# Optimization experiments

Hardware: AMD Instinct MI355X
Metric: run time of the kernel (lower is better)

## Reference

```python
import jax, jax.numpy as jnp
import numpy as np
import math

NUM_HEADS = 8
DIM_Q = 512
DIM_K = 512
DIM_V = 512
EPS = 1e-5


def _layernorm(x, g, b):
    mu = jnp.mean(x, axis=-1, keepdims=True)
    var = jnp.mean(jnp.square(x - mu), axis=-1, keepdims=True)
    return (x - mu) * jax.lax.rsqrt(var + EPS) * g + b


def setup_inputs() -> dict:
    key = jax.random.key(0)
    ks = jax.random.split(key, 16)
    B, Nq, Nk = 8, 1024, 1024
    s_q = 1.0 / math.sqrt(DIM_Q)
    s_v = 1.0 / math.sqrt(DIM_V)
    return {
        "Q": jax.random.normal(ks[0], (B, Nq, DIM_Q), jnp.float32),
        "K": jax.random.normal(ks[1], (B, Nk, DIM_K), jnp.float32),
        "Wq": jax.random.uniform(ks[2], (DIM_Q, DIM_V), jnp.float32, -s_q, s_q),
        "bq": jax.random.uniform(ks[3], (DIM_V,), jnp.float32, -s_q, s_q),
        "Wk": jax.random.uniform(ks[4], (DIM_K, DIM_V), jnp.float32, -s_q, s_q),
        "bk": jax.random.uniform(ks[5], (DIM_V,), jnp.float32, -s_q, s_q),
        "Wv": jax.random.uniform(ks[6], (DIM_K, DIM_V), jnp.float32, -s_q, s_q),
        "bv": jax.random.uniform(ks[7], (DIM_V,), jnp.float32, -s_q, s_q),
        "Wo": jax.random.uniform(ks[8], (DIM_V, DIM_V), jnp.float32, -s_v, s_v),
        "bo": jax.random.uniform(ks[9], (DIM_V,), jnp.float32, -s_v, s_v),
        "g0": jnp.ones((DIM_V,), jnp.float32),
        "b0": jnp.zeros((DIM_V,), jnp.float32),
        "g1": jnp.ones((DIM_V,), jnp.float32),
        "b1": jnp.zeros((DIM_V,), jnp.float32),
        "M": jax.random.randint(ks[10], (B, Nq, Nk), 0, 2, jnp.int32),
    }


def reference(Q, K, Wq, bq, Wk, bk, Wv, bv, Wo, bo, g0, b0, g1, b1, M):
    B, Nq, _ = Q.shape
    Nk = K.shape[1]
    H = NUM_HEADS
    d = DIM_V // H
    # projections
    Qp = Q @ Wq + bq                      # [B,Nq,Dv]
    Kp = K @ Wk + bk                      # [B,Nk,Dv]
    Vp = K @ Wv + bv                      # [B,Nk,Dv]
    # split heads: channel h*d+j -> head h (matches torch split/cat ordering)
    Qh = Qp.reshape(B, Nq, H, d)
    Kh = Kp.reshape(B, Nk, H, d)
    Vh = Vp.reshape(B, Nk, H, d)
    # scores scaled by sqrt(dim_V) (faithful to original, NOT sqrt(head_dim))
    A = jnp.einsum("bqhd,bkhd->bhqk", Qh, Kh) / math.sqrt(DIM_V)
    A = jnp.where(M[:, None, :, :] == 0, -jnp.inf, A)
    A = jax.nn.softmax(A, axis=-1)
    # residual add of the (projected, per-head) query, then merge heads
    O = Qh + jnp.einsum("bhqk,bkhd->bqhd", A, Vh)
    O = O.reshape(B, Nq, DIM_V)
    O = _layernorm(O, g0, b0)
    O = O + jax.nn.relu(O @ Wo + bo)
    O = _layernorm(O, g1, b1)
    return O
```

## Files before the change

kernel.cpp:

```cpp
#include <hip/hip_runtime.h>

typedef unsigned short u16;
typedef unsigned int u32;
typedef unsigned long long u64;
typedef __attribute__((ext_vector_type(8))) short short8;
typedef __attribute__((ext_vector_type(4))) float f32x4;
typedef __attribute__((ext_vector_type(4))) u32 u32x4;

#define BATCH 8
#define NSEQ 1024
#define DMODEL 512
#define HDIM 64
#define SCALE_LOG2E 0.06375871114929199f
#define FIXED_MAX 16.0f

#define O_QBF 0ULL
#define O_KBF 8388608ULL
#define O_WB  16777216ULL
#define O_QP  19922944ULL
#define O_KP  28311552ULL
#define O_VP  36700160ULL

__device__ __forceinline__ u16 f2bf(float f) {
  u32 u = __float_as_uint(f);
  u = (u + 0x7fffu + ((u >> 16) & 1u)) >> 16;
  return (u16)u;
}
__device__ __forceinline__ float bf2f(u16 s) {
  return __uint_as_float(((u32)s) << 16);
}
__device__ __forceinline__ void gload16(const void* g, void* l) {
  __builtin_amdgcn_global_load_lds((const __attribute__((address_space(1))) void*)g,
                                   (__attribute__((address_space(3))) void*)l, 16, 0, 0);
}
__device__ __forceinline__ u32 cvtpk(float a, float b) {
  u32 r;
  asm("v_cvt_pk_bf16_f32 %0, %1, %2" : "=v"(r) : "v"(a), "v"(b));
  return r;
}

__global__ __launch_bounds__(256) void prep_kernel(
    const float* __restrict__ Q, const float* __restrict__ K,
    const float* __restrict__ Wq, const float* __restrict__ Wk,
    const float* __restrict__ Wv, const float* __restrict__ Wo,
    const int* __restrict__ M,
    u16* __restrict__ Qbf, u16* __restrict__ Kbf, u16* __restrict__ Wb,
    u16* __restrict__ Mbias)
{
  __shared__ float lds[64 * 68];
  const int bi = blockIdx.x, t = threadIdx.x;
  if (bi < 4096) {
    const float* src = (bi < 2048) ? Q : K;
    u16* dst = (bi < 2048) ? Qbf : Kbf;
    const int lb = bi & 2047;
    const size_t base = ((size_t)lb * 256 + t) * 8;
    float4 a = *(const float4*)(src + base);
    float4 c = *(const float4*)(src + base + 4);
    short8 o;
    o[0] = (short)f2bf(a.x); o[1] = (short)f2bf(a.y);
    o[2] = (short)f2bf(a.z); o[3] = (short)f2bf(a.w);
    o[4] = (short)f2bf(c.x); o[5] = (short)f2bf(c.y);
    o[6] = (short)f2bf(c.z); o[7] = (short)f2bf(c.w);
    *(short8*)(dst + base) = o;
  } else if (bi < 4352) {
    const int qid = bi - 4096;
    const int w = qid >> 6;
    const int tt = qid & 63;
    const int tr = tt >> 3, tc = tt & 7;
    const float* W = (w == 0) ? Wq : (w == 1) ? Wk : (w == 2) ? Wv : Wo;
#pragma unroll
    for (int j = 0; j < 4; ++j) {
      int vi = j * 256 + t;
      int row = vi >> 4, c4 = vi & 15;
      float4 v = *(const float4*)(W + (size_t)(tr * 64 + row) * 512 + tc * 64 + c4 * 4);
      lds[row * 68 + c4 * 4 + 0] = v.x;
      lds[row * 68 + c4 * 4 + 1] = v.y;
      lds[row * 68 + c4 * 4 + 2] = v.z;
      lds[row * 68 + c4 * 4 + 3] = v.w;
    }
    __syncthreads();
#pragma unroll
    for (int j = 0; j < 2; ++j) {
      int oi = j * 256 + t;
      int nl = oi >> 3, k8 = oi & 7;
      short8 o;
#pragma unroll
      for (int i = 0; i < 8; ++i) o[i] = (short)f2bf(lds[(k8 * 8 + i) * 68 + nl]);
      *(short8*)(Wb + (size_t)w * 262144 + (size_t)(tc * 64 + nl) * 512 + tr * 64 + k8 * 8) = o;
    }
  } else {
    const int pb = bi - 4352;
    const size_t idx = ((size_t)pb * 256 + t) * 16;
    const int4* Ms = (const int4*)(M + idx);
    int4 m0 = Ms[0], m1 = Ms[1], m2 = Ms[2], m3 = Ms[3];
    int mv[16] = {m0.x, m0.y, m0.z, m0.w, m1.x, m1.y, m1.z, m1.w,
                  m2.x, m2.y, m2.z, m2.w, m3.x, m3.y, m3.z, m3.w};
    short8 o0, o1;
#pragma unroll
    for (int i = 0; i < 8; ++i) {
      o0[i] = mv[i] ? (short)0 : (short)0xC700;
      o1[i] = mv[8 + i] ? (short)0 : (short)0xC700;
    }
    *(short8*)(Mbias + idx) = o0;
    *(short8*)(Mbias + idx + 8) = o1;
  }
}

template<int MODE>
__global__ __launch_bounds__(256) void gemm_bt(
    const u16* __restrict__ Aq, const u16* __restrict__ Ak,
    const u16* __restrict__ Wb,
    const float* __restrict__ b0, const float* __restrict__ b1, const float* __restrict__ b2,
    u16* __restrict__ outp, const u16* __restrict__ resid)
{
  __shared__ __align__(16) char Alds[8192];
  __shared__ __align__(16) char Blds[8192];
  const int tid = threadIdx.x;
  const int wv = tid >> 6, lane = tid & 63;
  const int g16 = lane >> 4, l16 = lane & 15;
  const int wr = wv >> 1, wc = wv & 1;
  const int bx = blockIdx.x, by = blockIdx.y, bz = blockIdx.z;

  const u16* A; const u16* W; const float* bias; u16* out;
  if (MODE == 0) {
    A = (bz == 0) ? Aq : Ak;
    W = Wb + (size_t)bz * 262144;
    bias = (bz == 0) ? b0 : ((bz == 1) ? b1 : b2);
    out = outp + (size_t)bz * 4194304;
  } else {
    A = Aq; W = Wb; bias = b0; out = outp;
  }

  const int m0 = bx * 128, n0 = by * 128;
  f32x4 acc[4][4] = {};

  for (int kt = 0; kt < 16; ++kt) {
    const int k0 = kt * 32;
#pragma unroll
    for (int r = 0; r < 2; ++r) {
      int idx = r * 256 + tid;
      int row = idx >> 2, sl = idx & 3;
      gload16(A + (size_t)(m0 + row) * 512 + k0 + sl * 8, Alds + r * 4096 + wv * 1024);
      gload16(W + (size_t)(n0 + row) * 512 + k0 + sl * 8, Blds + r * 4096 + wv * 1024);
    }
    __syncthreads();
    short8 af[4], bfr[4];
#pragma unroll
    for (int mt = 0; mt < 4; ++mt)
      af[mt] = *(const short8*)(Alds + (wr * 64 + mt * 16 + l16) * 64 + g16 * 16);
#pragma unroll
    for (int nt = 0; nt < 4; ++nt)
      bfr[nt] = *(const short8*)(Blds + (wc * 64 + nt * 16 + l16) * 64 + g16 * 16);
#pragma unroll
    for (int mt = 0; mt < 4; ++mt)
#pragma unroll
      for (int nt = 0; nt < 4; ++nt)
        acc[mt][nt] = __builtin_amdgcn_mfma_f32_16x16x32_bf16(af[mt], bfr[nt], acc[mt][nt], 0, 0, 0);
    __syncthreads();
  }

#pragma unroll
  for (int nt = 0; nt < 4; ++nt) {
    int col = n0 + wc * 64 + nt * 16 + l16;
    float bcol = bias[col];
#pragma unroll
    for (int mt = 0; mt < 4; ++mt) {
#pragma unroll
      for (int r = 0; r < 4; ++r) {
        int row = m0 + wr * 64 + mt * 16 + g16 * 4 + r;
        float v = acc[mt][nt][r] + bcol;
        if (MODE == 1) {
          v = fmaxf(v, 0.f) + bf2f(resid[(size_t)row * 512 + col]);
        }
        out[(size_t)row * 512 + col] = f2bf(v);
      }
    }
  }
}

__global__ __launch_bounds__(256, 4) void attn_kernel(
    const u16* __restrict__ Qp, const u16* __restrict__ Kp, const u16* __restrict__ Vp,
    const u16* __restrict__ Mbias, u16* __restrict__ O1)
{
  __shared__ __align__(16) char K_lds[2][8192];
  __shared__ __align__(16) char VT_lds[2][8192];

  const int tid = threadIdx.x;
  const int wv = tid >> 6, lane = tid & 63;
  const int g16 = lane >> 4, l16 = lane & 15;
  const int l7 = l16 & 7;

  const int wg = blockIdx.x;
  const int swz = (wg & 7) * 128 + (wg >> 3);
  const int qt = swz & 15;
  const int h = (swz >> 4) & 7;
  const int b = swz >> 7;
  const int qg = qt * 64;
  const int hb = h * HDIM;
  const size_t batch_row = (size_t)b * NSEQ;

  const int q = qg + wv * 16 + l16;
  const int dv2 = (tid & 31) * 2;
  const int kg = tid >> 5;
  const int v_kc = kg >> 2, v_gg = kg & 3;

  short8 b_q[2];
#pragma unroll
  for (int c = 0; c < 2; ++c) {
    short8 raw = *(const short8*)(Qp + (batch_row + q) * DMODEL + hb + c * 32 + g16 * 8);
    short8 sc;
#pragma unroll
    for (int j = 0; j < 8; ++j) sc[j] = (short)f2bf(bf2f((u16)raw[j]) * SCALE_LOG2E);
    b_q[c] = sc;
  }

  const u64* Mq = (const u64*)(Mbias + (batch_row + q) * 1024);

  auto stageK = [&](int kt2, char* dst) {
#pragma unroll
    for (int r = 0; r < 2; ++r) {
      int idx = r * 256 + tid;
      int row = idx >> 3, sl = idx & 7;
      int chunk = sl ^ (row & 7);
      gload16(Kp + (batch_row + kt2 * 64 + row) * DMODEL + hb + chunk * 8,
              dst + r * 4096 + wv * 1024);
    }
  };
  auto loadV = [&](int kt2, u32 (&vr)[8]) {
#pragma unroll
    for (int j = 0; j < 8; ++j) {
      int row = v_kc * 32 + (j >> 2) * 16 + v_gg * 4 + (j & 3);
      vr[j] = *(const u32*)(Vp + (batch_row + kt2 * 64 + row) * DMODEL + hb + dv2);
    }
  };
  auto writeVT = [&](const u32 (&vr)[8], char* dstv) {
    u32x4 lo, hi;
#pragma unroll
    for (int i = 0; i < 4; ++i) {
      lo[i] = __builtin_amdgcn_perm(vr[2 * i + 1], vr[2 * i], 0x05040100u);
      hi[i] = __builtin_amdgcn_perm(vr[2 * i + 1], vr[2 * i], 0x07060302u);
    }
    *(u32x4*)(dstv + dv2 * 128 + ((kg ^ (dv2 & 7)) << 4)) = lo;
    *(u32x4*)(dstv + (dv2 + 1) * 128 + ((kg ^ ((dv2 + 1) & 7)) << 4)) = hi;
  };

  float lL = 0.f;
  f32x4 accO[4] = {};

  u32 vreg[8];
  u64 biasA[4], biasB[4];

  stageK(0, &K_lds[0][0]);
  loadV(0, vreg);
#pragma unroll
  for (int kf = 0; kf < 4; ++kf) biasA[kf] = Mq[kf * 4 + g16];
  writeVT(vreg, &VT_lds[0][0]);
  loadV(1, vreg);

#define ATTN_TILE(KT, CUR, BIN, BOUT)                                          \
  do {                                                                         \
    asm volatile("s_waitcnt vmcnt(12) lgkmcnt(0)" ::: "memory");               \
    __builtin_amdgcn_sched_barrier(0);                                         \
    __builtin_amdgcn_s_barrier();                                              \
    __builtin_amdgcn_sched_barrier(0);                                         \
    char* Kc = &K_lds[CUR][0];                                                 \
    char* Vc = &VT_lds[CUR][0];                                                \
    if ((KT) < 15) {                                                           \
      writeVT(vreg, &VT_lds[(CUR) ^ 1][0]);                                    \
      stageK((KT) + 1, &K_lds[(CUR) ^ 1][0]);                                  \
      loadV((KT) + 2 < 16 ? (KT) + 2 : 15, vreg);                              \
      _Pragma("unroll")                                                        \
      for (int kf = 0; kf < 4; ++kf)                                           \
        BOUT[kf] = Mq[((KT) + 1) * 16 + kf * 4 + g16];                         \
    }                                                                          \
    f32x4 s_[4];                                                               \
    __builtin_amdgcn_s_setprio(1);                                             \
    _Pragma("unroll")                                                          \
    for (int kf = 0; kf < 4; ++kf) {                                           \
      int row = kf * 16 + l16;                                                 \
      short8 ak0 = *(const short8*)(Kc + row * 128 + ((g16 ^ l7) << 4));       \
      short8 ak1 = *(const short8*)(Kc + row * 128 + (((4 + g16) ^ l7) << 4)); \
      u64 bv = BIN[kf];                                                        \
      u32 blo = (u32)bv, bhi = (u32)(bv >> 32);                                \
      f32x4 acc;                                                               \
      acc[0] = __uint_as_float(blo << 16);                                     \
      acc[1] = __uint_as_float(blo & 0xffff0000u);                             \
      acc[2] = __uint_as_float(bhi << 16);                                     \
      acc[3] = __uint_as_float(bhi & 0xffff0000u);                             \
      acc = __builtin_amdgcn_mfma_f32_16x16x32_bf16(ak0, b_q[0], acc, 0, 0, 0);\
      acc = __builtin_amdgcn_mfma_f32_16x16x32_bf16(ak1, b_q[1], acc, 0, 0, 0);\
      s_[kf] = acc;                                                            \
    }                                                                          \
    __builtin_amdgcn_s_setprio(0);                                             \
    float sum = 0.f;                                                           \
    u32 c0a[4], c1a[4];                                                        \
    _Pragma("unroll")                                                          \
    for (int kf = 0; kf < 4; ++kf) {                                           \
      float e0 = __builtin_amdgcn_exp2f(s_[kf][0] - FIXED_MAX);                \
      float e1 = __builtin_amdgcn_exp2f(s_[kf][1] - FIXED_MAX);                \
      float e2 = __builtin_amdgcn_exp2f(s_[kf][2] - FIXED_MAX);                \
      float e3 = __builtin_amdgcn_exp2f(s_[kf][3] - FIXED_MAX);                \
      sum += (e0 + e1) + (e2 + e3);                                            \
      c0a[kf] = cvtpk(e0, e1);                                                 \
      c1a[kf] = cvtpk(e2, e3);                                                 \
    }                                                                          \
    lL += sum;                                                                 \
    u32x4 t0 = {c0a[0], c1a[0], c0a[1], c1a[1]};                               \
    u32x4 t1 = {c0a[2], c1a[2], c0a[3], c1a[3]};                               \
    short8 b_p0 = *(short8*)&t0;                                               \
    short8 b_p1 = *(short8*)&t1;                                               \
    __builtin_amdgcn_s_setprio(1);                                             \
    _Pragma("unroll")                                                          \
    for (int f = 0; f < 4; ++f) {                                              \
      int vrow = f * 16 + l16;                                                 \
      short8 av0 = *(const short8*)(Vc + vrow * 128 + ((g16 ^ l7) << 4));      \
      short8 av1 = *(const short8*)(Vc + vrow * 128 + (((4 + g16) ^ l7) << 4));\
      accO[f] = __builtin_amdgcn_mfma_f32_16x16x32_bf16(av0, b_p0, accO[f], 0, 0, 0); \
      accO[f] = __builtin_amdgcn_mfma_f32_16x16x32_bf16(av1, b_p1, accO[f], 0, 0, 0); \
    }                                                                          \
    __builtin_amdgcn_s_setprio(0);                                             \
  } while (0)

  for (int t = 0; t < 8; ++t) {
    ATTN_TILE(2 * t, 0, biasA, biasB);
    ATTN_TILE(2 * t + 1, 1, biasB, biasA);
  }
#undef ATTN_TILE

  float l = lL;
  l += __shfl_xor(l, 16, 64);
  l += __shfl_xor(l, 32, 64);
  float inv = 1.0f / fmaxf(l, 1e-20f);
#pragma unroll
  for (int f = 0; f < 4; ++f) {
    size_t o = (batch_row + q) * DMODEL + hb + f * 16 + g16 * 4;
    u64 qh = *(const u64*)(Qp + o);
    u64 ov = 0;
#pragma unroll
    for (int r = 0; r < 4; ++r) {
      float val = accO[f][r] * inv + bf2f((u16)(qh >> (r * 16)));
      ov |= ((u64)f2bf(val)) << (r * 16);
    }
    *(u64*)(O1 + o) = ov;
  }
}

template<int OUTF>
__global__ __launch_bounds__(256) void ln_kernel(
    const u16* __restrict__ X, const float* __restrict__ g, const float* __restrict__ bb,
    void* __restrict__ outv)
{
  const int tid = threadIdx.x;
  const int wv = tid >> 6, lane = tid & 63;
  const size_t row = (size_t)blockIdx.x * 4 + wv;
  short8 x8 = *(const short8*)(X + row * 512 + lane * 8);
  float xf[8];
  float s = 0.f, s2 = 0.f;
#pragma unroll
  for (int i = 0; i < 8; ++i) {
    xf[i] = bf2f((u16)x8[i]);
    s += xf[i];
    s2 += xf[i] * xf[i];
  }
#pragma unroll
  for (int d = 1; d < 64; d <<= 1) {
    s += __shfl_xor(s, d, 64);
    s2 += __shfl_xor(s2, d, 64);
  }
  float mu = s * (1.f / 512.f);
  float var = s2 * (1.f / 512.f) - mu * mu;
  float rs = rsqrtf(var + 1e-5f);
  float4 ga = *(const float4*)(g + lane * 8);
  float4 gb = *(const float4*)(g + lane * 8 + 4);
  float4 ba = *(const float4*)(bb + lane * 8);
  float4 bc = *(const float4*)(bb + lane * 8 + 4);
  float gv[8] = {ga.x, ga.y, ga.z, ga.w, gb.x, gb.y, gb.z, gb.w};
  float bv[8] = {ba.x, ba.y, ba.z, ba.w, bc.x, bc.y, bc.z, bc.w};
  float y[8];
#pragma unroll
  for (int i = 0; i < 8; ++i) y[i] = (xf[i] - mu) * rs * gv[i] + bv[i];
  if (OUTF) {
    float* o = (float*)outv + row * 512 + lane * 8;
    float4 o1 = {y[0], y[1], y[2], y[3]};
    float4 o2 = {y[4], y[5], y[6], y[7]};
    *(float4*)o = o1;
    *(float4*)(o + 4) = o2;
  } else {
    short8 o;
#pragma unroll
    for (int i = 0; i < 8; ++i) o[i] = (short)f2bf(y[i]);
    *(short8*)((u16*)outv + row * 512 + lane * 8) = o;
  }
}

extern "C" void kernel_launch(void* const* d_in, const int* in_sizes, int n_in,
                              void* d_out, int out_size, void* d_ws, size_t ws_size,
                              hipStream_t stream) {
  (void)in_sizes; (void)n_in; (void)out_size; (void)ws_size;
  const float* Q  = (const float*)d_in[0];
  const float* K  = (const float*)d_in[1];
  const float* Wq = (const float*)d_in[2];
  const float* bq = (const float*)d_in[3];
  const float* Wk = (const float*)d_in[4];
  const float* bk = (const float*)d_in[5];
  const float* Wv = (const float*)d_in[6];
  const float* bv = (const float*)d_in[7];
  const float* Wo = (const float*)d_in[8];
  const float* bo = (const float*)d_in[9];
  const float* g0 = (const float*)d_in[10];
  const float* b0 = (const float*)d_in[11];
  const float* g1 = (const float*)d_in[12];
  const float* b1 = (const float*)d_in[13];
  const int*   M  = (const int*)d_in[14];
  float* out = (float*)d_out;
  char* ws = (char*)d_ws;

  u16* Qbf = (u16*)(ws + O_QBF);
  u16* Kbf = (u16*)(ws + O_KBF);
  u16* Wb  = (u16*)(ws + O_WB);
  u16* Qp  = (u16*)(ws + O_QP);
  u16* Kp  = (u16*)(ws + O_KP);
  u16* Vp  = (u16*)(ws + O_VP);
  u16* Mbias = (u16*)d_out;
  u16* O1  = Kbf;
  u16* Xn  = Qp;
  u16* Z   = Qbf;

  prep_kernel<<<6400, 256, 0, stream>>>(Q, K, Wq, Wk, Wv, Wo, M, Qbf, Kbf, Wb, Mbias);
  gemm_bt<0><<<dim3(64, 4, 3), 256, 0, stream>>>(Qbf, Kbf, Wb, bq, bk, bv, Qp, nullptr);
  attn_kernel<<<1024, 256, 0, stream>>>(Qp, Kp, Vp, Mbias, O1);
  ln_kernel<0><<<2048, 256, 0, stream>>>(O1, g0, b0, (void*)Xn);
  gemm_bt<1><<<dim3(64, 4, 1), 256, 0, stream>>>(Xn, nullptr, Wb + 3 * 262144, bo,
                                                 nullptr, nullptr, Z, Xn);
  ln_kernel<1><<<2048, 256, 0, stream>>>(Z, g1, b1, (void*)out);
}
```

Measured before the change: 118.4 us.

## Process two key tiles per barrier in attention with doubled LDS buffers

The attention loop now stages two 64-key K/V tiles per iteration into LDS buffers of twice the size. This halves the number of workgroup barriers and waitcnt points and lets more global loads sit in flight. In exchange, LDS per block doubles to 64KB, the launch-bounds occupancy hint drops from 4 to 2, and register use rises from the extra V staging registers and bias arrays, so fewer waves may be resident per CU.

```diff
diff --git a/kernel.cpp b/kernel.cpp
--- a/kernel.cpp
+++ b/kernel.cpp
@@ -178,12 +178,12 @@
   }
 }
 
-__global__ __launch_bounds__(256, 4) void attn_kernel(
+__global__ __launch_bounds__(256, 2) void attn_kernel(
     const u16* __restrict__ Qp, const u16* __restrict__ Kp, const u16* __restrict__ Vp,
     const u16* __restrict__ Mbias, u16* __restrict__ O1)
 {
-  __shared__ __align__(16) char K_lds[2][8192];
-  __shared__ __align__(16) char VT_lds[2][8192];
+  __shared__ __align__(16) char K_lds[2][16384];
+  __shared__ __align__(16) char VT_lds[2][16384];
 
   const int tid = threadIdx.x;
   const int wv = tid >> 6, lane = tid & 63;
@@ -247,40 +247,33 @@
   float lL = 0.f;
   f32x4 accO[4] = {};
 
-  u32 vreg[8];
-  u64 biasA[4], biasB[4];
+  u32 v0[8], v1[8];
+  u64 biasA[8], biasB[8];
 
   stageK(0, &K_lds[0][0]);
-  loadV(0, vreg);
-#pragma unroll
-  for (int kf = 0; kf < 4; ++kf) biasA[kf] = Mq[kf * 4 + g16];
-  writeVT(vreg, &VT_lds[0][0]);
-  loadV(1, vreg);
-
-#define ATTN_TILE(KT, CUR, BIN, BOUT)                                          \
+  stageK(1, &K_lds[0][8192]);
+  loadV(0, v0);
+  loadV(1, v1);
+#pragma unroll
+  for (int kf = 0; kf < 4; ++kf) {
+    biasA[kf] = Mq[kf * 4 + g16];
+    biasA[4 + kf] = Mq[16 + kf * 4 + g16];
+  }
+  writeVT(v0, &VT_lds[0][0]);
+  writeVT(v1, &VT_lds[0][8192]);
+  loadV(2, v0);
+  loadV(3, v1);
+
+#define SUBTILE(KCP, VCP, BARR, BOFF)                                          \
   do {                                                                         \
-    asm volatile("s_waitcnt vmcnt(12) lgkmcnt(0)" ::: "memory");               \
-    __builtin_amdgcn_sched_barrier(0);                                         \
-    __builtin_amdgcn_s_barrier();                                              \
-    __builtin_amdgcn_sched_barrier(0);                                         \
-    char* Kc = &K_lds[CUR][0];                                                 \
-    char* Vc = &VT_lds[CUR][0];                                                \
-    if ((KT) < 15) {                                                           \
-      writeVT(vreg, &VT_lds[(CUR) ^ 1][0]);                                    \
-      stageK((KT) + 1, &K_lds[(CUR) ^ 1][0]);                                  \
-      loadV((KT) + 2 < 16 ? (KT) + 2 : 15, vreg);                              \
-      _Pragma("unroll")                                                        \
-      for (int kf = 0; kf < 4; ++kf)                                           \
-        BOUT[kf] = Mq[((KT) + 1) * 16 + kf * 4 + g16];                         \
-    }                                                                          \
     f32x4 s_[4];                                                               \
     __builtin_amdgcn_s_setprio(1);                                             \
     _Pragma("unroll")                                                          \
     for (int kf = 0; kf < 4; ++kf) {                                           \
       int row = kf * 16 + l16;                                                 \
-      short8 ak0 = *(const short8*)(Kc + row * 128 + ((g16 ^ l7) << 4));       \
-      short8 ak1 = *(const short8*)(Kc + row * 128 + (((4 + g16) ^ l7) << 4)); \
-      u64 bv = BIN[kf];                                                        \
+      short8 ak0 = *(const short8*)((KCP) + row * 128 + ((g16 ^ l7) << 4));    \
+      short8 ak1 = *(const short8*)((KCP) + row * 128 + (((4 + g16) ^ l7) << 4)); \
+      u64 bv = BARR[(BOFF) + kf];                                              \
       u32 blo = (u32)bv, bhi = (u32)(bv >> 32);                                \
       f32x4 acc;                                                               \
       acc[0] = __uint_as_float(blo << 16);                                     \
@@ -313,19 +306,51 @@
     _Pragma("unroll")                                                          \
     for (int f = 0; f < 4; ++f) {                                              \
       int vrow = f * 16 + l16;                                                 \
-      short8 av0 = *(const short8*)(Vc + vrow * 128 + ((g16 ^ l7) << 4));      \
-      short8 av1 = *(const short8*)(Vc + vrow * 128 + (((4 + g16) ^ l7) << 4));\
+      short8 av0 = *(const short8*)((VCP) + vrow * 128 + ((g16 ^ l7) << 4));   \
+      short8 av1 = *(const short8*)((VCP) + vrow * 128 + (((4 + g16) ^ l7) << 4)); \
       accO[f] = __builtin_amdgcn_mfma_f32_16x16x32_bf16(av0, b_p0, accO[f], 0, 0, 0); \
       accO[f] = __builtin_amdgcn_mfma_f32_16x16x32_bf16(av1, b_p1, accO[f], 0, 0, 0); \
     }                                                                          \
     __builtin_amdgcn_s_setprio(0);                                             \
   } while (0)
 
-  for (int t = 0; t < 8; ++t) {
-    ATTN_TILE(2 * t, 0, biasA, biasB);
-    ATTN_TILE(2 * t + 1, 1, biasB, biasA);
-  }
-#undef ATTN_TILE
+#define ATTN_IT(IT, CUR, BIN, BOUT, VMCSTR)                                    \
+  do {                                                                         \
+    asm volatile("s_waitcnt vmcnt(" VMCSTR ") lgkmcnt(0)" ::: "memory");       \
+    __builtin_amdgcn_sched_barrier(0);                                         \
+    __builtin_amdgcn_s_barrier();                                              \
+    __builtin_amdgcn_sched_barrier(0);                                         \
+    char* Kc = &K_lds[CUR][0];                                                 \
+    char* Vc = &VT_lds[CUR][0];                                                \
+    if ((IT) < 7) {                                                            \
+      writeVT(v0, &VT_lds[(CUR) ^ 1][0]);                                      \
+      writeVT(v1, &VT_lds[(CUR) ^ 1][8192]);                                   \
+      stageK(2 * (IT) + 2, &K_lds[(CUR) ^ 1][0]);                              \
+      stageK(2 * (IT) + 3, &K_lds[(CUR) ^ 1][8192]);                           \
+    }                                                                          \
+    if ((IT) < 6) {                                                            \
+      loadV(2 * (IT) + 4, v0);                                                 \
+      loadV(2 * (IT) + 5, v1);                                                 \
+    }                                                                          \
+    if ((IT) < 7) {                                                            \
+      _Pragma("unroll")                                                        \
+      for (int kf = 0; kf < 4; ++kf) {                                         \
+        BOUT[kf] = Mq[(2 * (IT) + 2) * 16 + kf * 4 + g16];                     \
+        BOUT[4 + kf] = Mq[(2 * (IT) + 3) * 16 + kf * 4 + g16];                 \
+      }                                                                        \
+    }                                                                          \
+    SUBTILE(Kc, Vc, BIN, 0);                                                   \
+    SUBTILE(Kc + 8192, Vc + 8192, BIN, 4);                                     \
+  } while (0)
+
+  for (int t = 0; t < 3; ++t) {
+    ATTN_IT(2 * t, 0, biasA, biasB, "24");
+    ATTN_IT(2 * t + 1, 1, biasB, biasA, "24");
+  }
+  ATTN_IT(6, 0, biasA, biasB, "24");
+  ATTN_IT(7, 1, biasB, biasA, "8");
+#undef ATTN_IT
+#undef SUBTILE
 
   float l = lL;
   l += __shfl_xor(l, 16, 64);
```

New measurement: 117.1 us. No clear change (-1.1%).

## Pack attention mask into bitmask and remap GEMM blocks across XCDs

Applied to the files above, without the earlier changes.

The prep kernel now turns the int32 mask into a 1-bit-per-key bitmask via wave ballots, in place of a bf16 bias array the size of the full score matrix. The attention kernel reads one u64 per 64-key tile and expands the bits into the additive bias in registers. This cuts mask traffic in the attention kernel by a factor of 16 and shrinks the prep writes. The GEMM launches also become 1D with an XCD-aware block remap for better L2 locality. The cost is more per-element select work in the inner loop and a serial 32-iteration ballot loop per wave in prep.

```diff
diff --git a/kernel.cpp b/kernel.cpp
--- a/kernel.cpp
+++ b/kernel.cpp
@@ -17,6 +17,7 @@
 #define O_QBF 0ULL
 #define O_KBF 8388608ULL
 #define O_WB  16777216ULL
+#define O_MB  18874368ULL
 #define O_QP  19922944ULL
 #define O_KP  28311552ULL
 #define O_VP  36700160ULL
@@ -45,7 +46,7 @@
     const float* __restrict__ Wv, const float* __restrict__ Wo,
     const int* __restrict__ M,
     u16* __restrict__ Qbf, u16* __restrict__ Kbf, u16* __restrict__ Wb,
-    u16* __restrict__ Mbias)
+    u64* __restrict__ Mb)
 {
   __shared__ float lds[64 * 68];
   const int bi = blockIdx.x, t = threadIdx.x;
@@ -90,19 +91,16 @@
     }
   } else {
     const int pb = bi - 4352;
-    const size_t idx = ((size_t)pb * 256 + t) * 16;
-    const int4* Ms = (const int4*)(M + idx);
-    int4 m0 = Ms[0], m1 = Ms[1], m2 = Ms[2], m3 = Ms[3];
-    int mv[16] = {m0.x, m0.y, m0.z, m0.w, m1.x, m1.y, m1.z, m1.w,
-                  m2.x, m2.y, m2.z, m2.w, m3.x, m3.y, m3.z, m3.w};
-    short8 o0, o1;
-#pragma unroll
-    for (int i = 0; i < 8; ++i) {
-      o0[i] = mv[i] ? (short)0 : (short)0xC700;
-      o1[i] = mv[8 + i] ? (short)0 : (short)0xC700;
-    }
-    *(short8*)(Mbias + idx) = o0;
-    *(short8*)(Mbias + idx + 8) = o1;
+    const int wv = t >> 6, lane = t & 63;
+    for (int i = 0; i < 32; ++i) {
+      int widx = pb * 128 + wv * 32 + i;
+      int kc = widx & 15;
+      int qq = (widx >> 4) & 1023;
+      int bb = widx >> 14;
+      int mv = M[((size_t)bb * 1024 + qq) * 1024 + kc * 64 + lane];
+      u64 bal = __ballot(mv != 0);
+      if (lane == 0) Mb[widx] = bal;
+    }
   }
 }
 
@@ -119,7 +117,13 @@
   const int wv = tid >> 6, lane = tid & 63;
   const int g16 = lane >> 4, l16 = lane & 15;
   const int wr = wv >> 1, wc = wv & 1;
-  const int bx = blockIdx.x, by = blockIdx.y, bz = blockIdx.z;
+
+  const int p = blockIdx.x;
+  const int xcd = p & 7, rest = p >> 3;
+  const int bx = xcd + ((rest & 7) << 3);
+  const int q2 = rest >> 3;
+  const int by = (MODE == 0) ? (q2 & 3) : q2;
+  const int bz = (MODE == 0) ? (q2 >> 2) : 0;
 
   const u16* A; const u16* W; const float* bias; u16* out;
   if (MODE == 0) {
@@ -180,7 +184,7 @@
 
 __global__ __launch_bounds__(256, 4) void attn_kernel(
     const u16* __restrict__ Qp, const u16* __restrict__ Kp, const u16* __restrict__ Vp,
-    const u16* __restrict__ Mbias, u16* __restrict__ O1)
+    const u64* __restrict__ Mb, u16* __restrict__ O1)
 {
   __shared__ __align__(16) char K_lds[2][8192];
   __shared__ __align__(16) char VT_lds[2][8192];
@@ -214,7 +218,7 @@
     b_q[c] = sc;
   }
 
-  const u64* Mq = (const u64*)(Mbias + (batch_row + q) * 1024);
+  const u64* Mq = Mb + (batch_row + q) * 16;
 
   auto stageK = [&](int kt2, char* dst) {
 #pragma unroll
@@ -248,18 +252,17 @@
   f32x4 accO[4] = {};
 
   u32 vreg[8];
-  u64 biasA[4], biasB[4];
+  u64 mksA, mksB;
 
   stageK(0, &K_lds[0][0]);
   loadV(0, vreg);
-#pragma unroll
-  for (int kf = 0; kf < 4; ++kf) biasA[kf] = Mq[kf * 4 + g16];
+  mksA = Mq[0];
   writeVT(vreg, &VT_lds[0][0]);
   loadV(1, vreg);
 
-#define ATTN_TILE(KT, CUR, BIN, BOUT)                                          \
+#define ATTN_TILE(KT, CUR, MKS, MKSN)                                          \
   do {                                                                         \
-    asm volatile("s_waitcnt vmcnt(12) lgkmcnt(0)" ::: "memory");               \
+    asm volatile("s_waitcnt vmcnt(8) lgkmcnt(0)" ::: "memory");                \
     __builtin_amdgcn_sched_barrier(0);                                         \
     __builtin_amdgcn_s_barrier();                                              \
     __builtin_amdgcn_sched_barrier(0);                                         \
@@ -269,9 +272,7 @@
       writeVT(vreg, &VT_lds[(CUR) ^ 1][0]);                                    \
       stageK((KT) + 1, &K_lds[(CUR) ^ 1][0]);                                  \
       loadV((KT) + 2 < 16 ? (KT) + 2 : 15, vreg);                              \
-      _Pragma("unroll")                                                        \
-      for (int kf = 0; kf < 4; ++kf)                                           \
-        BOUT[kf] = Mq[((KT) + 1) * 16 + kf * 4 + g16];                         \
+      MKSN = Mq[(KT) + 1];                                                     \
     }                                                                          \
     f32x4 s_[4];                                                               \
     __builtin_amdgcn_s_setprio(1);                                             \
@@ -280,13 +281,12 @@
       int row = kf * 16 + l16;                                                 \
       short8 ak0 = *(const short8*)(Kc + row * 128 + ((g16 ^ l7) << 4));       \
       short8 ak1 = *(const short8*)(Kc + row * 128 + (((4 + g16) ^ l7) << 4)); \
-      u64 bv = BIN[kf];                                                        \
-      u32 blo = (u32)bv, bhi = (u32)(bv >> 32);                                \
+      u32 nib = ((u32)((MKS) >> (kf * 16 + g16 * 4))) & 15u;                   \
       f32x4 acc;                                                               \
-      acc[0] = __uint_as_float(blo << 16);                                     \
-      acc[1] = __uint_as_float(blo & 0xffff0000u);                             \
-      acc[2] = __uint_as_float(bhi << 16);                                     \
-      acc[3] = __uint_as_float(bhi & 0xffff0000u);                             \
+      acc[0] = (nib & 1u) ? 0.f : -32768.f;                                    \
+      acc[1] = (nib & 2u) ? 0.f : -32768.f;                                    \
+      acc[2] = (nib & 4u) ? 0.f : -32768.f;                                    \
+      acc[3] = (nib & 8u) ? 0.f : -32768.f;                                    \
       acc = __builtin_amdgcn_mfma_f32_16x16x32_bf16(ak0, b_q[0], acc, 0, 0, 0);\
       acc = __builtin_amdgcn_mfma_f32_16x16x32_bf16(ak1, b_q[1], acc, 0, 0, 0);\
       s_[kf] = acc;                                                            \
@@ -322,8 +322,8 @@
   } while (0)
 
   for (int t = 0; t < 8; ++t) {
-    ATTN_TILE(2 * t, 0, biasA, biasB);
-    ATTN_TILE(2 * t + 1, 1, biasB, biasA);
+    ATTN_TILE(2 * t, 0, mksA, mksB);
+    ATTN_TILE(2 * t + 1, 1, mksB, mksA);
   }
 #undef ATTN_TILE
 
@@ -418,19 +418,19 @@
   u16* Qbf = (u16*)(ws + O_QBF);
   u16* Kbf = (u16*)(ws + O_KBF);
   u16* Wb  = (u16*)(ws + O_WB);
+  u64* Mb  = (u64*)(ws + O_MB);
   u16* Qp  = (u16*)(ws + O_QP);
   u16* Kp  = (u16*)(ws + O_KP);
   u16* Vp  = (u16*)(ws + O_VP);
-  u16* Mbias = (u16*)d_out;
   u16* O1  = Kbf;
   u16* Xn  = Qp;
   u16* Z   = Qbf;
 
-  prep_kernel<<<6400, 256, 0, stream>>>(Q, K, Wq, Wk, Wv, Wo, M, Qbf, Kbf, Wb, Mbias);
-  gemm_bt<0><<<dim3(64, 4, 3), 256, 0, stream>>>(Qbf, Kbf, Wb, bq, bk, bv, Qp, nullptr);
-  attn_kernel<<<1024, 256, 0, stream>>>(Qp, Kp, Vp, Mbias, O1);
+  prep_kernel<<<5376, 256, 0, stream>>>(Q, K, Wq, Wk, Wv, Wo, M, Qbf, Kbf, Wb, Mb);
+  gemm_bt<0><<<768, 256, 0, stream>>>(Qbf, Kbf, Wb, bq, bk, bv, Qp, nullptr);
+  attn_kernel<<<1024, 256, 0, stream>>>(Qp, Kp, Vp, Mb, O1);
   ln_kernel<0><<<2048, 256, 0, stream>>>(O1, g0, b0, (void*)Xn);
-  gemm_bt<1><<<dim3(64, 4, 1), 256, 0, stream>>>(Xn, nullptr, Wb + 3 * 262144, bo,
-                                                 nullptr, nullptr, Z, Xn);
+  gemm_bt<1><<<256, 256, 0, stream>>>(Xn, nullptr, Wb + 3 * 262144, bo,
+                                      nullptr, nullptr, Z, Xn);
   ln_kernel<1><<<2048, 256, 0, stream>>>(Z, g1, b1, (void*)out);
 }
```

Measured after the change: 113.3 us. 1.05x faster.
